# Kernel optimization log

Measured on AMD Instinct MI355X. Metric: run time of the kernel, lower is better.

## Reference

```python
import jax, jax.numpy as jnp
import numpy as np

K = 20  # neighbors

def _graph_feature(x, k):
    # x: (B, N, 3) -> (B, 3, N, k) neighbor features (DGCNN-style gather)
    inner = -2.0 * jnp.einsum('bnd,bmd->bnm', x, x)
    xx = jnp.sum(x * x, axis=2, keepdims=True)              # (B, N, 1)
    pairwise = -xx - inner - jnp.swapaxes(xx, 1, 2)          # (B, N, N) = -||xi-xj||^2
    _, idx = jax.lax.top_k(pairwise, k)                      # (B, N, k) nearest neighbors
    feat = jax.vmap(lambda xb, ib: xb[ib])(x, idx)           # (B, N, k, 3)
    return jnp.transpose(feat, (0, 3, 1, 2))                 # (B, 3, N, k)

def _vn_layer(x, w, scale, shift):
    # matmul over channel dim, folded-BN affine, relu
    y = jnp.einsum('oc,bcnk->bonk', w, x)
    y = y * scale[None, :, None, None] + shift[None, :, None, None]
    return jax.nn.relu(y)

def setup_inputs() -> dict:
    key = jax.random.key(0)
    ks = jax.random.split(key, 12)
    B, N = 32, 256
    inp = {
        'x': jax.random.normal(ks[0], (B, N, 3), dtype=jnp.float32),
        'w1': jax.random.normal(ks[1], (64, 3), dtype=jnp.float32),
        's1': jnp.ones((64,), jnp.float32), 't1': jnp.zeros((64,), jnp.float32),
        'w2': jax.random.normal(ks[2], (128, 64), dtype=jnp.float32) * 0.1,
        's2': jnp.ones((128,), jnp.float32), 't2': jnp.zeros((128,), jnp.float32),
        'w3': jax.random.normal(ks[3], (256, 128), dtype=jnp.float32) * 0.1,
        's3': jnp.ones((256,), jnp.float32), 't3': jnp.zeros((256,), jnp.float32),
        'fc1_w': jax.random.normal(ks[4], (128, 256), dtype=jnp.float32) * 0.05,
        'fc1_b': jnp.zeros((128,), jnp.float32),
        'fc2_w': jax.random.normal(ks[5], (40, 128), dtype=jnp.float32) * 0.05,
        'fc2_b': jnp.zeros((40,), jnp.float32),
    }
    return inp

def reference(x, w1, s1, t1, w2, s2, t2, w3, s3, t3, fc1_w, fc1_b, fc2_w, fc2_b):
    h = _graph_feature(x, K)                                 # (B, 3, N, k)
    h = jax.nn.relu(_vn_layer(h, w1, s1, t1))                # double relu as in source
    h = jax.nn.relu(_vn_layer(h, w2, s2, t2))
    h = jax.nn.relu(_vn_layer(h, w3, s3, t3))                # (B, 256, N, k)
    h = jnp.max(h, axis=-1)                                  # (B, 256, N) with N==256
    h = jax.nn.relu(h @ fc1_w.T + fc1_b)                     # Linear over last axis
    return h @ fc2_w.T + fc2_b                               # (B, 256, 40)
```

## Files before the change

kernel.cpp:

```cpp
#include <hip/hip_runtime.h>
#include <hip/hip_bf16.h>

#define B_ 32
#define N_ 256
#define K_ 20
#define C1 64
#define C2 128
#define C3 256
#define F1 128
#define F2 40
#define NEG_INF (-3.402823466e38f)

__global__ __launch_bounds__(256) void k_front(const float* __restrict__ x,
    const float* __restrict__ w1, const float* __restrict__ s1, const float* __restrict__ b1,
    const float* __restrict__ w2, const float* __restrict__ s2, const float* __restrict__ b2,
    const float* __restrict__ w3, const float* __restrict__ s3, const float* __restrict__ b3,
    const float* __restrict__ fc1w,
    int* __restrict__ idx, float* __restrict__ P, float* __restrict__ fc1T) {

    __shared__ float smem[3136];
    const int blk = blockIdx.x;
    const int t   = threadIdx.x;

    if (blk < 512) {
        float* xs  = smem;
        float* y1t = smem + 64;
        float* y2t = smem + 1088;
        const int pbase = blk * 16;

        if (t < 48) xs[t] = x[(size_t)pbase * 3 + t];
        __syncthreads();

        {
            const int o = t & 63;
            const int q = t >> 6;
            const float wa = w1[o * 3 + 0], wb = w1[o * 3 + 1], wc = w1[o * 3 + 2];
            const float sc = s1[o], sh = b1[o];
            #pragma unroll
            for (int i = 0; i < 4; ++i) {
                const int p = q * 4 + i;
                float vv = wa * xs[p * 3 + 0] + wb * xs[p * 3 + 1] + wc * xs[p * 3 + 2];
                y1t[o * 16 + p] = fmaxf(vv * sc + sh, 0.0f);
            }
        }
        __syncthreads();

        {
            const int o = t & 127;
            const int h = (t >> 7) * 8;
            float acc[8] = {0, 0, 0, 0, 0, 0, 0, 0};
            const float4* wrow = (const float4*)(w2 + (size_t)o * C1);
            for (int c = 0; c < C1; c += 4) {
                float4 w4 = wrow[c >> 2];
                #pragma unroll
                for (int cc = 0; cc < 4; ++cc) {
                    const float wcc = (&w4.x)[cc];
                    const float* yp = y1t + (c + cc) * 16 + h;
                    #pragma unroll
                    for (int p = 0; p < 8; ++p) acc[p] += wcc * yp[p];
                }
            }
            const float sc = s2[o], sh = b2[o];
            #pragma unroll
            for (int p = 0; p < 8; ++p)
                y2t[o * 16 + h + p] = fmaxf(acc[p] * sc + sh, 0.0f);
        }
        __syncthreads();

        {
            const int o = t;
            float acc[16];
            #pragma unroll
            for (int p = 0; p < 16; ++p) acc[p] = 0.0f;
            const float4* wrow = (const float4*)(w3 + (size_t)o * C2);
            for (int c = 0; c < C2; c += 4) {
                float4 w4 = wrow[c >> 2];
                #pragma unroll
                for (int cc = 0; cc < 4; ++cc) {
                    const float wcc = (&w4.x)[cc];
                    const float* yp = y2t + (c + cc) * 16;
                    #pragma unroll
                    for (int p = 0; p < 16; ++p) acc[p] += wcc * yp[p];
                }
            }
            const float sc = s3[o], sh = b3[o];
            #pragma unroll
            for (int p = 0; p < 16; ++p) {
                float vv = fmaxf(acc[p] * sc + sh, 0.0f);
                P[(size_t)(pbase + p) * C3 + o] = vv;
            }
        }

    } else if (blk < 2560) {
        float* xs  = smem;
        float* xxs = smem + 768;
        const int tb   = blk - 512;
        const int lane = t & 63;
        const int wave = t >> 6;
        const int b    = tb >> 6;
        const int n    = ((tb & 63) << 2) | wave;
        const int bn   = (b << 8) | n;

        const float* xb = x + (size_t)b * N_ * 3;
        for (int e = t; e < N_ * 3; e += 256) xs[e] = xb[e];
        __syncthreads();
        {
            const float a0 = xs[t * 3 + 0], a1 = xs[t * 3 + 1], a2 = xs[t * 3 + 2];
            xxs[t] = a0 * a0 + a1 * a1 + a2 * a2;
        }
        __syncthreads();

        const float nx = xs[n * 3 + 0], ny = xs[n * 3 + 1], nz = xs[n * 3 + 2];
        const float xxn = xxs[n];

        unsigned long long k0, k1, k2, k3;
        {
            unsigned long long kk[4];
            #pragma unroll
            for (int i = 0; i < 4; ++i) {
                const int m = lane + (i << 6);
                const float cx = xs[m * 3 + 0], cy = xs[m * 3 + 1], cz = xs[m * 3 + 2];
                const float v = 2.0f * (nx * cx + ny * cy + nz * cz) - xxn - xxs[m];
                unsigned u = __float_as_uint(v);
                unsigned key32 = (u & 0x80000000u) ? ~u : (u | 0x80000000u);
                kk[i] = ((unsigned long long)key32 << 8) | (unsigned)(255 - m);
            }
            k0 = kk[0]; k1 = kk[1]; k2 = kk[2]; k3 = kk[3];
        }

        int mine = 0;
        #pragma unroll 1
        for (int it = 0; it < K_; ++it) {
            unsigned long long ra = (k0 > k1) ? k0 : k1;
            unsigned long long rb = (k2 > k3) ? k2 : k3;
            unsigned long long rk = (ra > rb) ? ra : rb;
            #pragma unroll
            for (int s = 1; s < 64; s <<= 1) {
                unsigned long long ok = __shfl_xor(rk, s, 64);
                if (ok > rk) rk = ok;
            }
            const int ri = 255 - (int)(rk & 0xFFull);
            if (lane == it) mine = ri;
            if (lane == (ri & 63)) {
                const int slot = ri >> 6;
                if      (slot == 0) k0 = 0ull;
                else if (slot == 1) k1 = 0ull;
                else if (slot == 2) k2 = 0ull;
                else                k3 = 0ull;
            }
        }
        if (lane < K_) idx[(size_t)bn * K_ + lane] = mine;

    } else {
        const int g = (blk - 2560) * 256 + t;
        #pragma unroll
        for (int i = 0; i < 8; ++i) {
            const int e = g + i * 4096;
            const int j = e >> 8, n = e & 255;
            fc1T[n * F1 + j] = fc1w[e];
        }
    }
}

__global__ __launch_bounds__(256) void k_gfc(const float* __restrict__ P,
                                             const int* __restrict__ idx,
                                             const float* __restrict__ fc1T,
                                             const float* __restrict__ fc1b,
                                             const float* __restrict__ fc2w,
                                             const float* __restrict__ fc2b,
                                             float* __restrict__ out) {
    const int b    = blockIdx.x >> 4;
    const int ch0  = (blockIdx.x & 15) * 16;
    const int t    = threadIdx.x;
    const int lane = t & 63;

    __shared__ float Ht[N_ * 16];
    __shared__ float gl[16 * 132];
    __shared__ float w2l[F2 * 129];

    for (int e = t; e < F2 * F1; e += 256)
        w2l[(e >> 7) * 129 + (e & 127)] = fc2w[e];

    {
        const int q  = t & 3;
        const int nl = t >> 2;
        const float* Pq = P + (size_t)b * N_ * C3 + ch0 + q * 4;
        #pragma unroll
        for (int r = 0; r < 4; ++r) {
            const int n = r * 64 + nl;
            const int* ib = idx + ((size_t)((b << 8) | n)) * K_;
            float4 m = make_float4(NEG_INF, NEG_INF, NEG_INF, NEG_INF);
            #pragma unroll
            for (int j = 0; j < K_; ++j) {
                const int id = ib[j];
                const float4 p = *(const float4*)(Pq + (size_t)id * C3);
                m.x = fmaxf(m.x, p.x);
                m.y = fmaxf(m.y, p.y);
                m.z = fmaxf(m.z, p.z);
                m.w = fmaxf(m.w, p.w);
            }
            *(float4*)&Ht[n * 16 + q * 4] = m;
        }
    }
    __syncthreads();

    {
        const int c0 = (t >> 6) * 4;
        float acc[2][4] = {};
        #pragma unroll 4
        for (int n = 0; n < N_; ++n) {
            const float2 w = *(const float2*)&fc1T[n * F1 + lane * 2];
            const float4 a = *(const float4*)&Ht[n * 16 + c0];
            #pragma unroll
            for (int c = 0; c < 4; ++c) {
                acc[0][c] += w.x * (&a.x)[c];
                acc[1][c] += w.y * (&a.x)[c];
            }
        }
        const float bb0 = fc1b[lane * 2], bb1 = fc1b[lane * 2 + 1];
        #pragma unroll
        for (int c = 0; c < 4; ++c) {
            float2 v;
            v.x = fmaxf(acc[0][c] + bb0, 0.0f);
            v.y = fmaxf(acc[1][c] + bb1, 0.0f);
            *(float2*)&gl[(c0 + c) * 132 + lane * 2] = v;
        }
    }
    __syncthreads();

    for (int o = t; o < 16 * F2; o += 256) {
        const int ci = o / F2;
        const int m  = o % F2;
        float acc = fc2b[m];
        const float* wr = w2l + m * 129;
        const float* gr = gl + ci * 132;
        #pragma unroll 4
        for (int j = 0; j < F1; ++j)
            acc += wr[j] * gr[j];
        out[((size_t)(b * C3 + ch0 + ci)) * F2 + m] = acc;
    }
}

extern "C" void kernel_launch(void* const* d_in, const int* in_sizes, int n_in,
                              void* d_out, int out_size, void* d_ws, size_t ws_size,
                              hipStream_t stream) {
    const float* x    = (const float*)d_in[0];
    const float* w1   = (const float*)d_in[1];
    const float* s1   = (const float*)d_in[2];
    const float* t1   = (const float*)d_in[3];
    const float* w2   = (const float*)d_in[4];
    const float* s2   = (const float*)d_in[5];
    const float* t2   = (const float*)d_in[6];
    const float* w3   = (const float*)d_in[7];
    const float* s3   = (const float*)d_in[8];
    const float* t3   = (const float*)d_in[9];
    const float* fc1w = (const float*)d_in[10];
    const float* fc1b = (const float*)d_in[11];
    const float* fc2w = (const float*)d_in[12];
    const float* fc2b = (const float*)d_in[13];
    float* out = (float*)d_out;

    char* ws = (char*)d_ws;
    int*   idx  = (int*)ws;
    float* P    = (float*)(ws + (size_t)B_ * N_ * K_ * 4);
    float* fc1T = P + (size_t)B_ * N_ * C3;

    k_front<<<2576, 256, 0, stream>>>(x, w1, s1, t1, w2, s2, t2, w3, s3, t3,
                                      fc1w, idx, P, fc1T);
    k_gfc<<<B_ * 16, 256, 0, stream>>>(P, idx, fc1T, fc1b, fc2w, fc2b, out);
}
```

Measured before the change: 152.5 us.

## Register-tile front MLP and speed up kNN selection with DPP 32-bit reduction

The per-point MLP stages are rewritten so each thread computes a small output-channel by point register tile with float4 LDS loads and vectorized stores to P. This cuts LDS traffic per FMA and makes the global writes coalesced. The kNN top-k loop now reduces 32-bit keys with DPP/swizzle instead of a 64-bit shuffle butterfly, then resolves the index with ballots and ffs, keeping lowest-index tie-breaking. The kNN blocks also read x directly from global and recompute squared norms, dropping the LDS staging and its barriers at the cost of redundant loads.

```diff
diff --git a/kernel.cpp b/kernel.cpp
--- a/kernel.cpp
+++ b/kernel.cpp
@@ -11,6 +11,28 @@
 #define F2 40
 #define NEG_INF (-3.402823466e38f)
 
+#define DPP_QUAD_XOR1 0xB1
+#define DPP_QUAD_XOR2 0x4E
+#define DPP_HALF_MIRR 0x141
+#define DPP_ROW_MIRR  0x140
+
+__device__ __forceinline__ unsigned wave_max_u32(unsigned v) {
+    unsigned m;
+    m = (unsigned)__builtin_amdgcn_update_dpp(0, (int)v, DPP_QUAD_XOR1, 0xF, 0xF, true);
+    v = m > v ? m : v;
+    m = (unsigned)__builtin_amdgcn_update_dpp(0, (int)v, DPP_QUAD_XOR2, 0xF, 0xF, true);
+    v = m > v ? m : v;
+    m = (unsigned)__builtin_amdgcn_update_dpp(0, (int)v, DPP_HALF_MIRR, 0xF, 0xF, true);
+    v = m > v ? m : v;
+    m = (unsigned)__builtin_amdgcn_update_dpp(0, (int)v, DPP_ROW_MIRR, 0xF, 0xF, true);
+    v = m > v ? m : v;
+    m = (unsigned)__builtin_amdgcn_ds_swizzle((int)v, 0x401F);
+    v = m > v ? m : v;
+    m = (unsigned)__shfl_xor((int)v, 32, 64);
+    v = m > v ? m : v;
+    return v;
+}
+
 __global__ __launch_bounds__(256) void k_front(const float* __restrict__ x,
     const float* __restrict__ w1, const float* __restrict__ s1, const float* __restrict__ b1,
     const float* __restrict__ w2, const float* __restrict__ s2, const float* __restrict__ b2,
@@ -19,111 +41,124 @@
     int* __restrict__ idx, float* __restrict__ P, float* __restrict__ fc1T) {
 
     __shared__ float smem[3136];
-    const int blk = blockIdx.x;
-    const int t   = threadIdx.x;
+    const int blk  = blockIdx.x;
+    const int t    = threadIdx.x;
+    const int lane = t & 63;
+    const int wv   = t >> 6;
 
     if (blk < 512) {
-        float* xs  = smem;
-        float* y1t = smem + 64;
-        float* y2t = smem + 1088;
+        float* xs = smem;
+        float* y1 = smem + 64;
+        float* y2 = smem + 1088;
         const int pbase = blk * 16;
+        const int p0 = wv * 4;
 
         if (t < 48) xs[t] = x[(size_t)pbase * 3 + t];
         __syncthreads();
 
         {
-            const int o = t & 63;
-            const int q = t >> 6;
-            const float wa = w1[o * 3 + 0], wb = w1[o * 3 + 1], wc = w1[o * 3 + 2];
-            const float sc = s1[o], sh = b1[o];
-            #pragma unroll
-            for (int i = 0; i < 4; ++i) {
-                const int p = q * 4 + i;
-                float vv = wa * xs[p * 3 + 0] + wb * xs[p * 3 + 1] + wc * xs[p * 3 + 2];
-                y1t[o * 16 + p] = fmaxf(vv * sc + sh, 0.0f);
-            }
+            const int oc = lane;
+            const float wa = w1[oc * 3 + 0], wb = w1[oc * 3 + 1], wc = w1[oc * 3 + 2];
+            const float sc = s1[oc], sh = b1[oc];
+            float4 v;
+            #pragma unroll
+            for (int p = 0; p < 4; ++p) {
+                const int pp = p0 + p;
+                float vv = wa * xs[pp * 3 + 0] + wb * xs[pp * 3 + 1] + wc * xs[pp * 3 + 2];
+                (&v.x)[p] = fmaxf(vv * sc + sh, 0.0f);
+            }
+            *(float4*)&y1[oc * 16 + p0] = v;
         }
         __syncthreads();
 
         {
-            const int o = t & 127;
-            const int h = (t >> 7) * 8;
-            float acc[8] = {0, 0, 0, 0, 0, 0, 0, 0};
-            const float4* wrow = (const float4*)(w2 + (size_t)o * C1);
-            for (int c = 0; c < C1; c += 4) {
-                float4 w4 = wrow[c >> 2];
-                #pragma unroll
-                for (int cc = 0; cc < 4; ++cc) {
-                    const float wcc = (&w4.x)[cc];
-                    const float* yp = y1t + (c + cc) * 16 + h;
+            float acc[2][4] = {};
+            const float4* wr0 = (const float4*)(w2 + (size_t)(lane * 2) * C1);
+            const float4* wr1 = (const float4*)(w2 + (size_t)(lane * 2 + 1) * C1);
+            for (int k = 0; k < C1; k += 4) {
+                float4 a[4];
+                #pragma unroll
+                for (int kk = 0; kk < 4; ++kk)
+                    a[kk] = *(const float4*)&y1[(k + kk) * 16 + p0];
+                const float4 wA = wr0[k >> 2];
+                const float4 wB = wr1[k >> 2];
+                #pragma unroll
+                for (int kk = 0; kk < 4; ++kk) {
                     #pragma unroll
-                    for (int p = 0; p < 8; ++p) acc[p] += wcc * yp[p];
+                    for (int p = 0; p < 4; ++p) {
+                        acc[0][p] += (&wA.x)[kk] * (&a[kk].x)[p];
+                        acc[1][p] += (&wB.x)[kk] * (&a[kk].x)[p];
+                    }
                 }
             }
-            const float sc = s2[o], sh = b2[o];
-            #pragma unroll
-            for (int p = 0; p < 8; ++p)
-                y2t[o * 16 + h + p] = fmaxf(acc[p] * sc + sh, 0.0f);
+            const float2 sc = *(const float2*)&s2[lane * 2];
+            const float2 sh = *(const float2*)&b2[lane * 2];
+            float4 v0, v1;
+            #pragma unroll
+            for (int p = 0; p < 4; ++p) {
+                (&v0.x)[p] = fmaxf(acc[0][p] * sc.x + sh.x, 0.0f);
+                (&v1.x)[p] = fmaxf(acc[1][p] * sc.y + sh.y, 0.0f);
+            }
+            *(float4*)&y2[(lane * 2) * 16 + p0]     = v0;
+            *(float4*)&y2[(lane * 2 + 1) * 16 + p0] = v1;
         }
         __syncthreads();
 
         {
-            const int o = t;
-            float acc[16];
-            #pragma unroll
-            for (int p = 0; p < 16; ++p) acc[p] = 0.0f;
-            const float4* wrow = (const float4*)(w3 + (size_t)o * C2);
-            for (int c = 0; c < C2; c += 4) {
-                float4 w4 = wrow[c >> 2];
-                #pragma unroll
-                for (int cc = 0; cc < 4; ++cc) {
-                    const float wcc = (&w4.x)[cc];
-                    const float* yp = y2t + (c + cc) * 16;
+            float acc[4][4] = {};
+            for (int k = 0; k < C2; k += 4) {
+                float4 a[4];
+                #pragma unroll
+                for (int kk = 0; kk < 4; ++kk)
+                    a[kk] = *(const float4*)&y2[(k + kk) * 16 + p0];
+                float4 w[4];
+                #pragma unroll
+                for (int o = 0; o < 4; ++o)
+                    w[o] = *(const float4*)(w3 + (size_t)(lane * 4 + o) * C2 + k);
+                #pragma unroll
+                for (int o = 0; o < 4; ++o) {
                     #pragma unroll
-                    for (int p = 0; p < 16; ++p) acc[p] += wcc * yp[p];
+                    for (int kk = 0; kk < 4; ++kk) {
+                        const float wvv = (&w[o].x)[kk];
+                        #pragma unroll
+                        for (int p = 0; p < 4; ++p)
+                            acc[o][p] += wvv * (&a[kk].x)[p];
+                    }
                 }
             }
-            const float sc = s3[o], sh = b3[o];
-            #pragma unroll
-            for (int p = 0; p < 16; ++p) {
-                float vv = fmaxf(acc[p] * sc + sh, 0.0f);
-                P[(size_t)(pbase + p) * C3 + o] = vv;
+            const float4 sc = *(const float4*)&s3[lane * 4];
+            const float4 sh = *(const float4*)&b3[lane * 4];
+            #pragma unroll
+            for (int p = 0; p < 4; ++p) {
+                float4 v;
+                #pragma unroll
+                for (int o = 0; o < 4; ++o)
+                    (&v.x)[o] = fmaxf(acc[o][p] * (&sc.x)[o] + (&sh.x)[o], 0.0f);
+                *(float4*)&P[(size_t)(pbase + p0 + p) * C3 + lane * 4] = v;
             }
         }
 
     } else if (blk < 2560) {
-        float* xs  = smem;
-        float* xxs = smem + 768;
-        const int tb   = blk - 512;
-        const int lane = t & 63;
-        const int wave = t >> 6;
-        const int b    = tb >> 6;
-        const int n    = ((tb & 63) << 2) | wave;
-        const int bn   = (b << 8) | n;
-
+        const int tb = blk - 512;
+        const int b  = tb >> 6;
+        const int n  = ((tb & 63) << 2) | wv;
+        const int bn = (b << 8) | n;
         const float* xb = x + (size_t)b * N_ * 3;
-        for (int e = t; e < N_ * 3; e += 256) xs[e] = xb[e];
-        __syncthreads();
+
+        const float nx = xb[n * 3 + 0], ny = xb[n * 3 + 1], nz = xb[n * 3 + 2];
+        const float xxn = nx * nx + ny * ny + nz * nz;
+
+        unsigned k0, k1, k2, k3;
         {
-            const float a0 = xs[t * 3 + 0], a1 = xs[t * 3 + 1], a2 = xs[t * 3 + 2];
-            xxs[t] = a0 * a0 + a1 * a1 + a2 * a2;
-        }
-        __syncthreads();
-
-        const float nx = xs[n * 3 + 0], ny = xs[n * 3 + 1], nz = xs[n * 3 + 2];
-        const float xxn = xxs[n];
-
-        unsigned long long k0, k1, k2, k3;
-        {
-            unsigned long long kk[4];
+            unsigned kk[4];
             #pragma unroll
             for (int i = 0; i < 4; ++i) {
                 const int m = lane + (i << 6);
-                const float cx = xs[m * 3 + 0], cy = xs[m * 3 + 1], cz = xs[m * 3 + 2];
-                const float v = 2.0f * (nx * cx + ny * cy + nz * cz) - xxn - xxs[m];
-                unsigned u = __float_as_uint(v);
-                unsigned key32 = (u & 0x80000000u) ? ~u : (u | 0x80000000u);
-                kk[i] = ((unsigned long long)key32 << 8) | (unsigned)(255 - m);
+                const float cx = xb[m * 3 + 0], cy = xb[m * 3 + 1], cz = xb[m * 3 + 2];
+                const float xxm = cx * cx + cy * cy + cz * cz;
+                const float v = 2.0f * (nx * cx + ny * cy + nz * cz) - xxn - xxm;
+                const unsigned u = __float_as_uint(v);
+                kk[i] = (u & 0x80000000u) ? ~u : (u | 0x80000000u);
             }
             k0 = kk[0]; k1 = kk[1]; k2 = kk[2]; k3 = kk[3];
         }
@@ -131,22 +166,25 @@
         int mine = 0;
         #pragma unroll 1
         for (int it = 0; it < K_; ++it) {
-            unsigned long long ra = (k0 > k1) ? k0 : k1;
-            unsigned long long rb = (k2 > k3) ? k2 : k3;
-            unsigned long long rk = (ra > rb) ? ra : rb;
-            #pragma unroll
-            for (int s = 1; s < 64; s <<= 1) {
-                unsigned long long ok = __shfl_xor(rk, s, 64);
-                if (ok > rk) rk = ok;
-            }
-            const int ri = 255 - (int)(rk & 0xFFull);
+            unsigned ra = k0 > k1 ? k0 : k1;
+            unsigned rb = k2 > k3 ? k2 : k3;
+            const unsigned M = wave_max_u32(ra > rb ? ra : rb);
+            const unsigned long long b0 = __ballot(k0 == M);
+            const unsigned long long b1 = __ballot(k1 == M);
+            const unsigned long long b2m = __ballot(k2 == M);
+            const unsigned long long b3m = __ballot(k3 == M);
+            int ri;
+            if      (b0)  ri = __ffsll((long long)b0) - 1;
+            else if (b1)  ri = 64  + __ffsll((long long)b1) - 1;
+            else if (b2m) ri = 128 + __ffsll((long long)b2m) - 1;
+            else          ri = 192 + __ffsll((long long)b3m) - 1;
             if (lane == it) mine = ri;
             if (lane == (ri & 63)) {
                 const int slot = ri >> 6;
-                if      (slot == 0) k0 = 0ull;
-                else if (slot == 1) k1 = 0ull;
-                else if (slot == 2) k2 = 0ull;
-                else                k3 = 0ull;
+                if      (slot == 0) k0 = 0u;
+                else if (slot == 1) k1 = 0u;
+                else if (slot == 2) k2 = 0u;
+                else                k3 = 0u;
             }
         }
         if (lane < K_) idx[(size_t)bn * K_ + lane] = mine;
```

Result: slower. 162.8 us (+6.8%).
